# Kernel tuning notes

Measured on AMD Instinct MI355X. Metric: run time of the kernel, lower is better.

## Reference

```python
import jax, jax.numpy as jnp
import numpy as np

B, N, L = 64, 256, 1024
OUT = L // 2   # ChebConv out_channels = Seq_len / 2
ALPHA = 0.5    # DirGNNConv default alpha


def _glorot(key, shape):
    # PyG ChebConv lins use glorot init
    lim = float(np.sqrt(6.0 / (shape[0] + shape[1])))
    return jax.random.uniform(key, shape, minval=-lim, maxval=lim, dtype=jnp.float32)


def setup_inputs() -> dict:
    key = jax.random.key(0)
    ks = jax.random.split(key, 8)
    x = jax.random.normal(ks[0], (B, N, L), dtype=jnp.float32)
    # dense per-sample adjacency; only used via nonzero() in torch, never enters math (K=1)
    At = jax.random.randint(ks[1], (B, N, N), 0, 2, dtype=jnp.int32)
    W_in = _glorot(ks[2], (L, OUT))
    b_in = jnp.zeros((OUT,), dtype=jnp.float32)
    W_out = _glorot(ks[3], (L, OUT))
    b_out = jnp.zeros((OUT,), dtype=jnp.float32)
    # DirGNNConv root Linear (kaiming-ish uniform; exact init irrelevant for correctness baseline)
    lim = float(1.0 / np.sqrt(L))
    W_root = jax.random.uniform(ks[4], (L, OUT), minval=-lim, maxval=lim, dtype=jnp.float32)
    b_root = jax.random.uniform(ks[5], (OUT,), minval=-lim, maxval=lim, dtype=jnp.float32)
    return {"x": x, "At": At, "W_in": W_in, "b_in": b_in,
            "W_out": W_out, "b_out": b_out, "W_root": W_root, "b_root": b_root}


def reference(x, At, W_in, b_in, W_out, b_out, W_root, b_root):
    # so the batched edge_index built from At.nonzero() never influences the output.
    # DirGNNConv: alpha * conv_out(x) + (1-alpha) * conv_in(x) + root_lin(x).
    xf = x.reshape(B * N, L)                        # [B*N, L]
    y = (ALPHA * (xf @ W_out + b_out)
         + (1.0 - ALPHA) * (xf @ W_in + b_in)
         + (xf @ W_root + b_root))                  # [B*N, OUT]
    return y.reshape(B, N, OUT)
```

## Files before the change

### kernel.cpp

```cpp
#include <hip/hip_runtime.h>
#include <stdint.h>

static constexpr int Mrows = 16384;
static constexpr int Kdim  = 1024;
static constexpr int Ncols = 512;

typedef __attribute__((ext_vector_type(8))) short bf16x8;
typedef __attribute__((ext_vector_type(4))) float f32x4;

__device__ __forceinline__ unsigned short f2bf(float f) {
  unsigned u = __builtin_bit_cast(unsigned, f);
  u += 0x7FFFu + ((u >> 16) & 1u);
  return (unsigned short)(u >> 16);
}
__device__ __forceinline__ unsigned f2bf2(float lo, float hi) {
  unsigned ul = __builtin_bit_cast(unsigned, lo);
  unsigned uh = __builtin_bit_cast(unsigned, hi);
  ul += 0x7FFFu + ((ul >> 16) & 1u);
  uh += 0x7FFFu + ((uh >> 16) & 1u);
  return (ul >> 16) | (uh & 0xFFFF0000u);
}

__device__ __forceinline__ void gl2lds16(const void* g, void* l) {
  __builtin_amdgcn_global_load_lds(
      (const __attribute__((address_space(1))) void*)g,
      (__attribute__((address_space(3))) void*)l, 16, 0, 0);
}

__global__ __launch_bounds__(256) void prep(
    const float* __restrict__ x,
    const float* __restrict__ Win, const float* __restrict__ Wout,
    const float* __restrict__ Wroot,
    unsigned short* __restrict__ Xbf, unsigned short* __restrict__ Wt)
{
  const int bid = blockIdx.x;
  const int t = threadIdx.x;
  if (bid < 8192) {
    const size_t base = ((size_t)bid * 256 + t) * 8;
    const float4 v0 = *(const float4*)(x + base);
    const float4 v1 = *(const float4*)(x + base + 4);
    uint4 p;
    p.x = f2bf2(v0.x, v0.y); p.y = f2bf2(v0.z, v0.w);
    p.z = f2bf2(v1.x, v1.y); p.w = f2bf2(v1.z, v1.w);
    *(uint4*)(Xbf + base) = p;
  } else {
    __shared__ unsigned short lds[32 * 36];
    const int b2 = bid - 8192;
    const int tk0 = (b2 & 31) * 32;
    const int tn0 = (b2 >> 5) * 32;
    {
      const int k  = t >> 3;
      const int nq = (t & 7) * 4;
      const int gi = (tk0 + k) * Ncols + tn0 + nq;
      const float4 wi = *(const float4*)(Win + gi);
      const float4 wo = *(const float4*)(Wout + gi);
      const float4 wr = *(const float4*)(Wroot + gi);
      lds[(nq + 0) * 36 + k] = f2bf(0.5f * (wi.x + wo.x) + wr.x);
      lds[(nq + 1) * 36 + k] = f2bf(0.5f * (wi.y + wo.y) + wr.y);
      lds[(nq + 2) * 36 + k] = f2bf(0.5f * (wi.z + wo.z) + wr.z);
      lds[(nq + 3) * 36 + k] = f2bf(0.5f * (wi.w + wo.w) + wr.w);
    }
    __syncthreads();
    {
      const int n  = t >> 3;
      const int k8 = (t & 7) * 4;
      const ushort4 v = *(const ushort4*)&lds[n * 36 + k8];
      *(ushort4*)(Wt + (size_t)(tn0 + n) * Kdim + tk0 + k8) = v;
    }
  }
}

__global__ __launch_bounds__(256, 2) void gemm_bf16(
    const unsigned short* __restrict__ Xbf, const unsigned short* __restrict__ Wt,
    const float* __restrict__ b_in, const float* __restrict__ b_out,
    const float* __restrict__ b_root, float* __restrict__ Y)
{
  __shared__ __attribute__((aligned(16))) short As[128 * 32];
  __shared__ __attribute__((aligned(16))) short Bs[128 * 32];

  const int bid = blockIdx.x;
  const int m0 = (bid & 127) * 128;
  const int n0 = (bid >> 7) * 128;

  const int t    = threadIdx.x;
  const int lane = t & 63;
  const int w    = t >> 6;
  const int wm   = w >> 1;
  const int wn   = w & 1;
  const int quad = lane >> 4;
  const int lm   = lane & 15;

  const int sr = lane >> 2;
  const int ss = lane & 3;
  const int sc = ss ^ ((sr >> 1) & 3);
  const unsigned short* gA = Xbf + (size_t)(m0 + w * 32 + sr) * Kdim + sc * 8;
  const unsigned short* gB = Wt  + (size_t)(n0 + w * 32 + sr) * Kdim + sc * 8;
  short* const lA0 = &As[(w * 32) * 32];
  short* const lA1 = &As[(w * 32 + 16) * 32];
  short* const lB0 = &Bs[(w * 32) * 32];
  short* const lB1 = &Bs[(w * 32 + 16) * 32];
  const int rowK = 16 * Kdim;

  const int slot = quad ^ ((lm >> 1) & 3);
  const int aoff = (wm * 64 + lm) * 32 + slot * 8;
  const int boff = (wn * 64 + lm) * 32 + slot * 8;

  f32x4 acc[4][4] = {};

  #pragma unroll 1
  for (int it = 0; it < 32; ++it) {
    const unsigned short* ga = gA + it * 32;
    const unsigned short* gb = gB + it * 32;
    gl2lds16(ga,        lA0);
    gl2lds16(ga + rowK, lA1);
    gl2lds16(gb,        lB0);
    gl2lds16(gb + rowK, lB1);
    __syncthreads();

    bf16x8 af[4], bfr[4];
    #pragma unroll
    for (int i = 0; i < 4; ++i) af[i]  = *(const bf16x8*)&As[aoff + i * 16 * 32];
    #pragma unroll
    for (int j = 0; j < 4; ++j) bfr[j] = *(const bf16x8*)&Bs[boff + j * 16 * 32];

    #pragma unroll
    for (int i = 0; i < 4; ++i)
      #pragma unroll
      for (int j = 0; j < 4; ++j)
        acc[i][j] = __builtin_amdgcn_mfma_f32_16x16x32_bf16(af[i], bfr[j], acc[i][j], 0, 0, 0);

    __syncthreads();
  }

  #pragma unroll
  for (int j = 0; j < 4; ++j) {
    const int gc = n0 + wn * 64 + j * 16 + lm;
    const float bias = 0.5f * (b_in[gc] + b_out[gc]) + b_root[gc];
    #pragma unroll
    for (int i = 0; i < 4; ++i) {
      const int gr = m0 + wm * 64 + i * 16 + quad * 4;
      float* yp = Y + (size_t)gr * Ncols + gc;
      #pragma unroll
      for (int r = 0; r < 4; ++r)
        yp[(size_t)r * Ncols] = acc[i][j][r] + bias;
    }
  }
}

extern "C" void kernel_launch(void* const* d_in, const int* in_sizes, int n_in,
                              void* d_out, int out_size, void* d_ws, size_t ws_size,
                              hipStream_t stream)
{
  const float* x      = (const float*)d_in[0];
  const float* W_in   = (const float*)d_in[2];
  const float* b_in   = (const float*)d_in[3];
  const float* W_out  = (const float*)d_in[4];
  const float* b_out  = (const float*)d_in[5];
  const float* W_root = (const float*)d_in[6];
  const float* b_root = (const float*)d_in[7];
  float* y = (float*)d_out;

  unsigned short* Xbf = (unsigned short*)d_ws;
  unsigned short* Wt  = (unsigned short*)d_ws + (size_t)Mrows * Kdim;

  prep<<<dim3(8192 + 512), dim3(256), 0, stream>>>(x, W_in, W_out, W_root, Xbf, Wt);
  gemm_bf16<<<dim3(512), dim3(256), 0, stream>>>(Xbf, Wt, b_in, b_out, b_root, y);
}
```

Before: 155.4 us.

## Fuse x fp32-to-bf16 conversion into GEMM A-tile loading with register prefetch

Removes the separate pass that converted x to a bf16 workspace. The GEMM now loads fp32 x directly into registers, converts it to bf16 and stores it into LDS, and prefetches the next K-slice during the MFMA work. This avoids writing and re-reading a 32 MB intermediate. In exchange the GEMM reads twice as many bytes for A, since x is re-read per N-tile (4 times) at fp32. The trailing barrier is replaced with an lgkmcnt wait plus a raw s_barrier.

```diff
diff --git a/kernel.cpp b/kernel.cpp
--- a/kernel.cpp
+++ b/kernel.cpp
@@ -27,51 +27,38 @@
       (__attribute__((address_space(3))) void*)l, 16, 0, 0);
 }
 
-__global__ __launch_bounds__(256) void prep(
-    const float* __restrict__ x,
+__global__ __launch_bounds__(256) void prep_w(
     const float* __restrict__ Win, const float* __restrict__ Wout,
-    const float* __restrict__ Wroot,
-    unsigned short* __restrict__ Xbf, unsigned short* __restrict__ Wt)
+    const float* __restrict__ Wroot, unsigned short* __restrict__ Wt)
 {
-  const int bid = blockIdx.x;
-  const int t = threadIdx.x;
-  if (bid < 8192) {
-    const size_t base = ((size_t)bid * 256 + t) * 8;
-    const float4 v0 = *(const float4*)(x + base);
-    const float4 v1 = *(const float4*)(x + base + 4);
-    uint4 p;
-    p.x = f2bf2(v0.x, v0.y); p.y = f2bf2(v0.z, v0.w);
-    p.z = f2bf2(v1.x, v1.y); p.w = f2bf2(v1.z, v1.w);
-    *(uint4*)(Xbf + base) = p;
-  } else {
-    __shared__ unsigned short lds[32 * 36];
-    const int b2 = bid - 8192;
-    const int tk0 = (b2 & 31) * 32;
-    const int tn0 = (b2 >> 5) * 32;
-    {
-      const int k  = t >> 3;
-      const int nq = (t & 7) * 4;
-      const int gi = (tk0 + k) * Ncols + tn0 + nq;
-      const float4 wi = *(const float4*)(Win + gi);
-      const float4 wo = *(const float4*)(Wout + gi);
-      const float4 wr = *(const float4*)(Wroot + gi);
-      lds[(nq + 0) * 36 + k] = f2bf(0.5f * (wi.x + wo.x) + wr.x);
-      lds[(nq + 1) * 36 + k] = f2bf(0.5f * (wi.y + wo.y) + wr.y);
-      lds[(nq + 2) * 36 + k] = f2bf(0.5f * (wi.z + wo.z) + wr.z);
-      lds[(nq + 3) * 36 + k] = f2bf(0.5f * (wi.w + wo.w) + wr.w);
-    }
-    __syncthreads();
-    {
-      const int n  = t >> 3;
-      const int k8 = (t & 7) * 4;
-      const ushort4 v = *(const ushort4*)&lds[n * 36 + k8];
-      *(ushort4*)(Wt + (size_t)(tn0 + n) * Kdim + tk0 + k8) = v;
-    }
+  __shared__ unsigned short lds[32 * 36];
+  const int t  = threadIdx.x;
+  const int b2 = blockIdx.x;
+  const int tk0 = (b2 & 31) * 32;
+  const int tn0 = (b2 >> 5) * 32;
+  {
+    const int k  = t >> 3;
+    const int nq = (t & 7) * 4;
+    const int gi = (tk0 + k) * Ncols + tn0 + nq;
+    const float4 wi = *(const float4*)(Win + gi);
+    const float4 wo = *(const float4*)(Wout + gi);
+    const float4 wr = *(const float4*)(Wroot + gi);
+    lds[(nq + 0) * 36 + k] = f2bf(0.5f * (wi.x + wo.x) + wr.x);
+    lds[(nq + 1) * 36 + k] = f2bf(0.5f * (wi.y + wo.y) + wr.y);
+    lds[(nq + 2) * 36 + k] = f2bf(0.5f * (wi.z + wo.z) + wr.z);
+    lds[(nq + 3) * 36 + k] = f2bf(0.5f * (wi.w + wo.w) + wr.w);
+  }
+  __syncthreads();
+  {
+    const int n  = t >> 3;
+    const int k8 = (t & 7) * 4;
+    const ushort4 v = *(const ushort4*)&lds[n * 36 + k8];
+    *(ushort4*)(Wt + (size_t)(tn0 + n) * Kdim + tk0 + k8) = v;
   }
 }
 
-__global__ __launch_bounds__(256, 2) void gemm_bf16(
-    const unsigned short* __restrict__ Xbf, const unsigned short* __restrict__ Wt,
+__global__ __launch_bounds__(256, 2) void gemm_fused(
+    const float* __restrict__ x, const unsigned short* __restrict__ Wt,
     const float* __restrict__ b_in, const float* __restrict__ b_out,
     const float* __restrict__ b_root, float* __restrict__ Y)
 {
@@ -93,10 +80,10 @@
   const int sr = lane >> 2;
   const int ss = lane & 3;
   const int sc = ss ^ ((sr >> 1) & 3);
-  const unsigned short* gA = Xbf + (size_t)(m0 + w * 32 + sr) * Kdim + sc * 8;
-  const unsigned short* gB = Wt  + (size_t)(n0 + w * 32 + sr) * Kdim + sc * 8;
-  short* const lA0 = &As[(w * 32) * 32];
-  short* const lA1 = &As[(w * 32 + 16) * 32];
+  const float* gX          = x  + (size_t)(m0 + w * 32 + sr) * Kdim + sc * 8;
+  const unsigned short* gB = Wt + (size_t)(n0 + w * 32 + sr) * Kdim + sc * 8;
+  short* const lA0 = &As[(w * 32 + sr) * 32 + ss * 8];
+  short* const lA1 = lA0 + 16 * 32;
   short* const lB0 = &Bs[(w * 32) * 32];
   short* const lB1 = &Bs[(w * 32 + 16) * 32];
   const int rowK = 16 * Kdim;
@@ -107,14 +94,24 @@
 
   f32x4 acc[4][4] = {};
 
+  float4 a00 = *(const float4*)(gX);
+  float4 a01 = *(const float4*)(gX + 4);
+  float4 a10 = *(const float4*)(gX + rowK);
+  float4 a11 = *(const float4*)(gX + rowK + 4);
+
   #pragma unroll 1
   for (int it = 0; it < 32; ++it) {
-    const unsigned short* ga = gA + it * 32;
-    const unsigned short* gb = gB + it * 32;
-    gl2lds16(ga,        lA0);
-    gl2lds16(ga + rowK, lA1);
-    gl2lds16(gb,        lB0);
-    gl2lds16(gb + rowK, lB1);
+    gl2lds16(gB + it * 32,        lB0);
+    gl2lds16(gB + it * 32 + rowK, lB1);
+
+    uint4 pa, pb;
+    pa.x = f2bf2(a00.x, a00.y); pa.y = f2bf2(a00.z, a00.w);
+    pa.z = f2bf2(a01.x, a01.y); pa.w = f2bf2(a01.z, a01.w);
+    pb.x = f2bf2(a10.x, a10.y); pb.y = f2bf2(a10.z, a10.w);
+    pb.z = f2bf2(a11.x, a11.y); pb.w = f2bf2(a11.z, a11.w);
+    *(uint4*)lA0 = pa;
+    *(uint4*)lA1 = pb;
+
     __syncthreads();
 
     bf16x8 af[4], bfr[4];
@@ -123,13 +120,22 @@
     #pragma unroll
     for (int j = 0; j < 4; ++j) bfr[j] = *(const bf16x8*)&Bs[boff + j * 16 * 32];
 
+    if (it < 31) {
+      const float* gx = gX + (it + 1) * 32;
+      a00 = *(const float4*)(gx);
+      a01 = *(const float4*)(gx + 4);
+      a10 = *(const float4*)(gx + rowK);
+      a11 = *(const float4*)(gx + rowK + 4);
+    }
+
     #pragma unroll
     for (int i = 0; i < 4; ++i)
       #pragma unroll
       for (int j = 0; j < 4; ++j)
         acc[i][j] = __builtin_amdgcn_mfma_f32_16x16x32_bf16(af[i], bfr[j], acc[i][j], 0, 0, 0);
 
-    __syncthreads();
+    asm volatile("s_waitcnt lgkmcnt(0)" ::: "memory");
+    __builtin_amdgcn_s_barrier();
   }
 
   #pragma unroll
@@ -160,9 +166,8 @@
   const float* b_root = (const float*)d_in[7];
   float* y = (float*)d_out;
 
-  unsigned short* Xbf = (unsigned short*)d_ws;
-  unsigned short* Wt  = (unsigned short*)d_ws + (size_t)Mrows * Kdim;
+  unsigned short* Wt = (unsigned short*)d_ws;
 
-  prep<<<dim3(8192 + 512), dim3(256), 0, stream>>>(x, W_in, W_out, W_root, Xbf, Wt);
-  gemm_bf16<<<dim3(512), dim3(256), 0, stream>>>(Xbf, Wt, b_in, b_out, b_root, y);
+  prep_w<<<dim3(512), dim3(256), 0, stream>>>(W_in, W_out, W_root, Wt);
+  gemm_fused<<<dim3(512), dim3(256), 0, stream>>>(x, Wt, b_in, b_out, b_root, y);
 }
```

Result: no change. 157.9 us (+1.6%).

## Pre-pack swizzled X tiles and triple-buffer GEMM K-loop with smaller tiles

Applied to the files above, without the earlier changes.

The prep kernel now writes X as bf16 in a per-tile, pre-swizzled layout, so each GEMM wave loads its A tile with one contiguous 16-byte-per-lane load. The GEMM shrinks its M tile to 64 rows, doubles the grid to 1024 blocks with an XCD-aware block mapping, and raises the occupancy hint to 4 blocks per CU. It also replaces the two-barrier load-then-compute loop with a 3-stage LDS ring using partial vmcnt waits, so global loads overlap the MFMAs. The cost is more B-tile reloads, since each W tile is now shared by only 64 rows, and the prep kernel's strided scatter writes are less coalesced.

```diff
diff --git a/kernel.cpp b/kernel.cpp
--- a/kernel.cpp
+++ b/kernel.cpp
@@ -4,6 +4,13 @@
 static constexpr int Mrows = 16384;
 static constexpr int Kdim  = 1024;
 static constexpr int Ncols = 512;
+
+static constexpr int TM  = 64;
+static constexpr int TN  = 128;
+static constexpr int BK  = 32;
+static constexpr int NMT = Mrows / TM;
+static constexpr int NNT = Ncols / TN;
+static constexpr int NKT = Kdim / BK;
 
 typedef __attribute__((ext_vector_type(8))) short bf16x8;
 typedef __attribute__((ext_vector_type(4))) float f32x4;
@@ -31,21 +38,35 @@
     const float* __restrict__ x,
     const float* __restrict__ Win, const float* __restrict__ Wout,
     const float* __restrict__ Wroot,
-    unsigned short* __restrict__ Xbf, unsigned short* __restrict__ Wt)
+    unsigned short* __restrict__ Xpack, unsigned short* __restrict__ Wt)
 {
   const int bid = blockIdx.x;
   const int t = threadIdx.x;
-  if (bid < 8192) {
-    const size_t base = ((size_t)bid * 256 + t) * 8;
-    const float4 v0 = *(const float4*)(x + base);
-    const float4 v1 = *(const float4*)(x + base + 4);
-    uint4 p;
-    p.x = f2bf2(v0.x, v0.y); p.y = f2bf2(v0.z, v0.w);
-    p.z = f2bf2(v1.x, v1.y); p.w = f2bf2(v1.z, v1.w);
-    *(uint4*)(Xbf + base) = p;
+  if (bid < 512) {
+    const int mt = bid >> 1;
+    const int h  = bid & 1;
+    const float* xrow0 = x + (size_t)bid * 32 * Kdim;
+    unsigned short* img0 = Xpack + (size_t)mt * NKT * 2048;
+    #pragma unroll
+    for (int j = 0; j < 16; ++j) {
+      const int p  = j * 256 + t;
+      const int rr = p >> 7;
+      const int q  = p & 127;
+      const int kt = q >> 2;
+      const int c  = q & 3;
+      const int ri = h * 32 + rr;
+      const int s  = c ^ ((rr >> 1) & 3);
+      const float* src = xrow0 + (size_t)rr * Kdim + q * 8;
+      const float4 lo = *(const float4*)(src);
+      const float4 hi = *(const float4*)(src + 4);
+      uint4 pk;
+      pk.x = f2bf2(lo.x, lo.y); pk.y = f2bf2(lo.z, lo.w);
+      pk.z = f2bf2(hi.x, hi.y); pk.w = f2bf2(hi.z, hi.w);
+      *(uint4*)(img0 + (size_t)kt * 2048 + ri * 32 + s * 8) = pk;
+    }
   } else {
     __shared__ unsigned short lds[32 * 36];
-    const int b2 = bid - 8192;
+    const int b2 = bid - 512;
     const int tk0 = (b2 & 31) * 32;
     const int tn0 = (b2 >> 5) * 32;
     {
@@ -70,17 +91,23 @@
   }
 }
 
-__global__ __launch_bounds__(256, 2) void gemm_bf16(
-    const unsigned short* __restrict__ Xbf, const unsigned short* __restrict__ Wt,
+__global__ __launch_bounds__(256, 4) void gemm_bf16(
+    const unsigned short* __restrict__ Xpack, const unsigned short* __restrict__ Wt,
     const float* __restrict__ b_in, const float* __restrict__ b_out,
     const float* __restrict__ b_root, float* __restrict__ Y)
 {
-  __shared__ __attribute__((aligned(16))) short As[128 * 32];
-  __shared__ __attribute__((aligned(16))) short Bs[128 * 32];
-
-  const int bid = blockIdx.x;
-  const int m0 = (bid & 127) * 128;
-  const int n0 = (bid >> 7) * 128;
+  constexpr int ABUF = TM * BK;
+  constexpr int BBUF = TN * BK;
+  __shared__ __attribute__((aligned(16))) short As[3 * ABUF];
+  __shared__ __attribute__((aligned(16))) short Bs[3 * BBUF];
+
+  const int bid  = blockIdx.x;
+  const int xcd  = bid & 7;
+  const int slot = bid >> 3;
+  const int nt   = slot & 3;
+  const int mt   = xcd * 32 + (slot >> 2);
+  const int m0   = mt * TM;
+  const int n0   = nt * TN;
 
   const int t    = threadIdx.x;
   const int lane = t & 63;
@@ -90,55 +117,71 @@
   const int quad = lane >> 4;
   const int lm   = lane & 15;
 
+  const unsigned short* gA = Xpack + (size_t)mt * NKT * 2048 + w * 512 + lane * 8;
+  short* const lA = &As[w * 512];
+
   const int sr = lane >> 2;
   const int ss = lane & 3;
   const int sc = ss ^ ((sr >> 1) & 3);
-  const unsigned short* gA = Xbf + (size_t)(m0 + w * 32 + sr) * Kdim + sc * 8;
-  const unsigned short* gB = Wt  + (size_t)(n0 + w * 32 + sr) * Kdim + sc * 8;
-  short* const lA0 = &As[(w * 32) * 32];
-  short* const lA1 = &As[(w * 32 + 16) * 32];
+  const unsigned short* gB = Wt + (size_t)(n0 + w * 32 + sr) * Kdim + sc * 8;
   short* const lB0 = &Bs[(w * 32) * 32];
-  short* const lB1 = &Bs[(w * 32 + 16) * 32];
+  short* const lB1 = lB0 + 16 * 32;
   const int rowK = 16 * Kdim;
 
-  const int slot = quad ^ ((lm >> 1) & 3);
-  const int aoff = (wm * 64 + lm) * 32 + slot * 8;
-  const int boff = (wn * 64 + lm) * 32 + slot * 8;
-
-  f32x4 acc[4][4] = {};
-
+  const int fslot = quad ^ ((lm >> 1) & 3);
+  const int aoff = (wm * 32 + lm) * 32 + fslot * 8;
+  const int boff = (wn * 64 + lm) * 32 + fslot * 8;
+
+  f32x4 acc[2][4] = {};
+
+#define STAGE(TT, BUF) do {                                               \
+    gl2lds16(gA + (size_t)(TT) * 2048, lA + (BUF) * ABUF);                \
+    gl2lds16(gB + (TT) * 32,        lB0 + (BUF) * BBUF);                  \
+    gl2lds16(gB + (TT) * 32 + rowK, lB1 + (BUF) * BBUF);                  \
+  } while (0)
+
+#define COMPUTE(BUF) do {                                                 \
+    bf16x8 af[2], bfr[4];                                                 \
+    _Pragma("unroll") for (int i = 0; i < 2; ++i)                         \
+      af[i]  = *(const bf16x8*)&As[(BUF) * ABUF + aoff + i * 512];        \
+    _Pragma("unroll") for (int j = 0; j < 4; ++j)                         \
+      bfr[j] = *(const bf16x8*)&Bs[(BUF) * BBUF + boff + j * 512];        \
+    _Pragma("unroll") for (int i = 0; i < 2; ++i)                         \
+      _Pragma("unroll") for (int j = 0; j < 4; ++j)                       \
+        acc[i][j] = __builtin_amdgcn_mfma_f32_16x16x32_bf16(              \
+            af[i], bfr[j], acc[i][j], 0, 0, 0);                           \
+  } while (0)
+
+  STAGE(0, 0);
+  STAGE(1, 1);
+  asm volatile("s_waitcnt vmcnt(3)" ::: "memory");
+  __builtin_amdgcn_s_barrier();
+
+  int b0 = 0, b1 = 1, b2 = 2;
   #pragma unroll 1
-  for (int it = 0; it < 32; ++it) {
-    const unsigned short* ga = gA + it * 32;
-    const unsigned short* gb = gB + it * 32;
-    gl2lds16(ga,        lA0);
-    gl2lds16(ga + rowK, lA1);
-    gl2lds16(gb,        lB0);
-    gl2lds16(gb + rowK, lB1);
-    __syncthreads();
-
-    bf16x8 af[4], bfr[4];
-    #pragma unroll
-    for (int i = 0; i < 4; ++i) af[i]  = *(const bf16x8*)&As[aoff + i * 16 * 32];
-    #pragma unroll
-    for (int j = 0; j < 4; ++j) bfr[j] = *(const bf16x8*)&Bs[boff + j * 16 * 32];
-
-    #pragma unroll
-    for (int i = 0; i < 4; ++i)
-      #pragma unroll
-      for (int j = 0; j < 4; ++j)
-        acc[i][j] = __builtin_amdgcn_mfma_f32_16x16x32_bf16(af[i], bfr[j], acc[i][j], 0, 0, 0);
-
-    __syncthreads();
+  for (int it = 0; it < 30; ++it) {
+    STAGE(it + 2, b2);
+    __builtin_amdgcn_sched_barrier(0);
+    COMPUTE(b0);
+    asm volatile("s_waitcnt vmcnt(3)" ::: "memory");
+    __builtin_amdgcn_s_barrier();
+    const int tmp = b0; b0 = b1; b1 = b2; b2 = tmp;
   }
+  COMPUTE(b0);
+  asm volatile("s_waitcnt vmcnt(0)" ::: "memory");
+  __builtin_amdgcn_s_barrier();
+  COMPUTE(b1);
+
+#undef COMPUTE
+#undef STAGE
 
   #pragma unroll
   for (int j = 0; j < 4; ++j) {
     const int gc = n0 + wn * 64 + j * 16 + lm;
     const float bias = 0.5f * (b_in[gc] + b_out[gc]) + b_root[gc];
     #pragma unroll
-    for (int i = 0; i < 4; ++i) {
-      const int gr = m0 + wm * 64 + i * 16 + quad * 4;
+    for (int i = 0; i < 2; ++i) {
+      const int gr = m0 + wm * 32 + i * 16 + quad * 4;
       float* yp = Y + (size_t)gr * Ncols + gc;
       #pragma unroll
       for (int r = 0; r < 4; ++r)
@@ -160,9 +203,9 @@
   const float* b_root = (const float*)d_in[7];
   float* y = (float*)d_out;
 
-  unsigned short* Xbf = (unsigned short*)d_ws;
-  unsigned short* Wt  = (unsigned short*)d_ws + (size_t)Mrows * Kdim;
-
-  prep<<<dim3(8192 + 512), dim3(256), 0, stream>>>(x, W_in, W_out, W_root, Xbf, Wt);
-  gemm_bf16<<<dim3(512), dim3(256), 0, stream>>>(Xbf, Wt, b_in, b_out, b_root, y);
-}
+  unsigned short* Xpack = (unsigned short*)d_ws;
+  unsigned short* Wt = (unsigned short*)d_ws + (size_t)Mrows * Kdim;
+
+  prep<<<dim3(1024), dim3(256), 0, stream>>>(x, W_in, W_out, W_root, Xpack, Wt);
+  gemm_bf16<<<dim3(1024), dim3(256), 0, stream>>>(Xpack, Wt, b_in, b_out, b_root, y);
+}
```

Result: no change. 155.6 us (+0.1%).

## Restructure GEMM with triple-buffered LDS A tiles and register-direct B loads

Applied to the files above, without the earlier changes.

The GEMM block tile changes from 128x128 to 64 rows by 256 columns. Each wave now loads its B (weight) fragments straight from global memory into registers, double-buffered one k-step ahead. A tiles are staged through a three-deep LDS ring filled two k-steps ahead. The two __syncthreads per iteration become a single barrier with a partial vmcnt wait, so loads overlap the MFMA work. The cost is more registers and uncoalesced 16-byte global reads of B per lane, and correctness depends on a hand-tuned vmcnt count.

```diff
diff --git a/kernel.cpp b/kernel.cpp
--- a/kernel.cpp
+++ b/kernel.cpp
@@ -70,75 +70,95 @@
   }
 }
 
-__global__ __launch_bounds__(256, 2) void gemm_bf16(
+__global__ __launch_bounds__(256, 2) void gemm_hyb(
     const unsigned short* __restrict__ Xbf, const unsigned short* __restrict__ Wt,
     const float* __restrict__ b_in, const float* __restrict__ b_out,
     const float* __restrict__ b_root, float* __restrict__ Y)
 {
-  __shared__ __attribute__((aligned(16))) short As[128 * 32];
-  __shared__ __attribute__((aligned(16))) short Bs[128 * 32];
+  constexpr int ABUF = 64 * 32;
+  __shared__ __attribute__((aligned(16))) short As[3 * ABUF];
 
   const int bid = blockIdx.x;
-  const int m0 = (bid & 127) * 128;
-  const int n0 = (bid >> 7) * 128;
+  const int m0  = (bid >> 1) * 64;
+  const int nh  = bid & 1;
 
   const int t    = threadIdx.x;
   const int lane = t & 63;
   const int w    = t >> 6;
-  const int wm   = w >> 1;
-  const int wn   = w & 1;
   const int quad = lane >> 4;
   const int lm   = lane & 15;
+  const int nw   = nh * 256 + w * 64;
 
   const int sr = lane >> 2;
   const int ss = lane & 3;
   const int sc = ss ^ ((sr >> 1) & 3);
-  const unsigned short* gA = Xbf + (size_t)(m0 + w * 32 + sr) * Kdim + sc * 8;
-  const unsigned short* gB = Wt  + (size_t)(n0 + w * 32 + sr) * Kdim + sc * 8;
-  short* const lA0 = &As[(w * 32) * 32];
-  short* const lA1 = &As[(w * 32 + 16) * 32];
-  short* const lB0 = &Bs[(w * 32) * 32];
-  short* const lB1 = &Bs[(w * 32 + 16) * 32];
-  const int rowK = 16 * Kdim;
+  const unsigned short* gA = Xbf + (size_t)(m0 + w * 16 + sr) * Kdim + sc * 8;
+  short* const lA = &As[w * 512];
 
-  const int slot = quad ^ ((lm >> 1) & 3);
-  const int aoff = (wm * 64 + lm) * 32 + slot * 8;
-  const int boff = (wn * 64 + lm) * 32 + slot * 8;
+  const unsigned short* gB = Wt + (size_t)(nw + lm) * Kdim + quad * 8;
+  constexpr size_t BROW = (size_t)16 * Kdim;
+
+  const int aoff = lm * 32 + (quad ^ ((lm >> 1) & 3)) * 8;
 
   f32x4 acc[4][4] = {};
+  bf16x8 PB0, PB1, PB2, PB3, QB0, QB1, QB2, QB3;
 
+#define LOADB(S, KK) do {                                                 \
+    const unsigned short* b_ = gB + (size_t)(KK) * 32;                    \
+    S##B0 = *(const bf16x8*)(b_);                                         \
+    S##B1 = *(const bf16x8*)(b_ + BROW);                                  \
+    S##B2 = *(const bf16x8*)(b_ + 2 * BROW);                              \
+    S##B3 = *(const bf16x8*)(b_ + 3 * BROW);                              \
+  } while (0)
+
+#define BODY(TT, S, R) do {                                               \
+                \
+    { int ta_ = (TT) + 2; if (ta_ > 31) ta_ = 31;                         \
+      gl2lds16(gA + ta_ * 32, lA + b2_ * ABUF); }                         \
+    __builtin_amdgcn_sched_barrier(0);                                    \
+    { int tb_ = (TT) + 1; if (tb_ > 31) tb_ = 31;                         \
+      LOADB(R, tb_); }                                                    \
+    bf16x8 af[4];                                                         \
+    _Pragma("unroll") for (int i = 0; i < 4; ++i)                         \
+      af[i] = *(const bf16x8*)&As[b0_ * ABUF + aoff + i * 512];           \
+    _Pragma("unroll") for (int i = 0; i < 4; ++i) {                       \
+      acc[i][0] = __builtin_amdgcn_mfma_f32_16x16x32_bf16(af[i], S##B0, acc[i][0], 0, 0, 0); \
+      acc[i][1] = __builtin_amdgcn_mfma_f32_16x16x32_bf16(af[i], S##B1, acc[i][1], 0, 0, 0); \
+      acc[i][2] = __builtin_amdgcn_mfma_f32_16x16x32_bf16(af[i], S##B2, acc[i][2], 0, 0, 0); \
+      acc[i][3] = __builtin_amdgcn_mfma_f32_16x16x32_bf16(af[i], S##B3, acc[i][3], 0, 0, 0); \
+    }                                                                     \
+    asm volatile("s_waitcnt vmcnt(5)" ::: "memory");                      \
+    __builtin_amdgcn_s_barrier();                                         \
+    __builtin_amdgcn_sched_barrier(0);                                    \
+    { const int r_ = b0_; b0_ = b1_; b1_ = b2_; b2_ = r_; }               \
+  } while (0)
+
+  gl2lds16(gA,      lA);
+  gl2lds16(gA + 32, lA + ABUF);
+  __builtin_amdgcn_sched_barrier(0);
+  LOADB(P, 0);
+  asm volatile("s_waitcnt vmcnt(5)" ::: "memory");
+  __builtin_amdgcn_s_barrier();
+  __builtin_amdgcn_sched_barrier(0);
+
+  int b0_ = 0, b1_ = 1, b2_ = 2;
   #pragma unroll 1
-  for (int it = 0; it < 32; ++it) {
-    const unsigned short* ga = gA + it * 32;
-    const unsigned short* gb = gB + it * 32;
-    gl2lds16(ga,        lA0);
-    gl2lds16(ga + rowK, lA1);
-    gl2lds16(gb,        lB0);
-    gl2lds16(gb + rowK, lB1);
-    __syncthreads();
+  for (int it = 0; it < 32; it += 2) {
+    BODY(it,     P, Q);
+    BODY(it + 1, Q, P);
+  }
+  asm volatile("s_waitcnt vmcnt(0)" ::: "memory");
 
-    bf16x8 af[4], bfr[4];
-    #pragma unroll
-    for (int i = 0; i < 4; ++i) af[i]  = *(const bf16x8*)&As[aoff + i * 16 * 32];
-    #pragma unroll
-    for (int j = 0; j < 4; ++j) bfr[j] = *(const bf16x8*)&Bs[boff + j * 16 * 32];
-
-    #pragma unroll
-    for (int i = 0; i < 4; ++i)
-      #pragma unroll
-      for (int j = 0; j < 4; ++j)
-        acc[i][j] = __builtin_amdgcn_mfma_f32_16x16x32_bf16(af[i], bfr[j], acc[i][j], 0, 0, 0);
-
-    __syncthreads();
-  }
+#undef BODY
+#undef LOADB
 
   #pragma unroll
   for (int j = 0; j < 4; ++j) {
-    const int gc = n0 + wn * 64 + j * 16 + lm;
+    const int gc = nw + j * 16 + lm;
     const float bias = 0.5f * (b_in[gc] + b_out[gc]) + b_root[gc];
     #pragma unroll
     for (int i = 0; i < 4; ++i) {
-      const int gr = m0 + wm * 64 + i * 16 + quad * 4;
+      const int gr = m0 + i * 16 + quad * 4;
       float* yp = Y + (size_t)gr * Ncols + gc;
       #pragma unroll
       for (int r = 0; r < 4; ++r)
@@ -164,5 +184,5 @@
   unsigned short* Wt  = (unsigned short*)d_ws + (size_t)Mrows * Kdim;
 
   prep<<<dim3(8192 + 512), dim3(256), 0, stream>>>(x, W_in, W_out, W_root, Xbf, Wt);
-  gemm_bf16<<<dim3(512), dim3(256), 0, stream>>>(Xbf, Wt, b_in, b_out, b_root, y);
+  gemm_hyb<<<dim3(512), dim3(256), 0, stream>>>(Xbf, Wt, b_in, b_out, b_root, y);
 }
```

After: 166.8 us. +7.4%, slower.
